# Kernel tuning notes

Hardware: AMD Instinct MI355X
Metric: run time of the kernel (lower is better)

## Reference

```python
import jax, jax.numpy as jnp
import numpy as np

B, D, QL, DL, E, V, NB = 32, 8, 16, 512, 300, 50000, 5
EPS = 1e-8  # torch cosine_similarity eps
# numpy.histogram edges [-1.0,-0.5,0,0.5,1.0,1.0] -> 5 bins, last bin [1.0,1.0] inclusive
BIN_LO = jnp.array([-1.0, -0.5, 0.0, 0.5, 1.0], dtype=jnp.float32)
BIN_HI = jnp.array([-0.5, 0.0, 0.5, 1.0, 1.0], dtype=jnp.float32)


def setup_inputs() -> dict:
    key = jax.random.key(0)
    ks = jax.random.split(key, 12)
    batch_queries = jax.random.randint(ks[0], (B, QL), 0, V)
    query_len = jax.random.randint(ks[1], (B,), 1, QL)
    batch_docs = jax.random.randint(ks[2], (B, D, DL), 0, V)
    doc_len = jax.random.randint(ks[3], (B, D), 1, DL)
    emb = jax.random.normal(ks[4], (V, E), dtype=jnp.float32) * 0.1
    emb = emb.at[0].set(0.0)  # PAD row (padding_idx)
    w_g = jax.random.normal(ks[5], (E, 1), dtype=jnp.float32) * 0.05
    b_g = jnp.zeros((1,), dtype=jnp.float32)
    w1 = jax.random.normal(ks[6], (NB, 1), dtype=jnp.float32) * 0.3
    b1 = jnp.zeros((1,), dtype=jnp.float32)
    w2 = jax.random.normal(ks[7], (1, 1), dtype=jnp.float32)
    b2 = jnp.zeros((1,), dtype=jnp.float32)
    w_o = jax.random.normal(ks[8], (1, 1), dtype=jnp.float32)
    b_o = jnp.zeros((1,), dtype=jnp.float32)
    return {"batch_queries": batch_queries, "query_len": query_len,
            "batch_docs": batch_docs, "doc_len": doc_len,
            "emb": emb, "w_g": w_g, "b_g": b_g, "w1": w1, "b1": b1,
            "w2": w2, "b2": b2, "w_o": w_o, "b_o": b_o}


def _histogram(cos):
    # cos: [N, qlen, dlen] -> counts [N, qlen, 5] (numpy.histogram semantics)
    v = cos[..., None]                              # [N,q,d,1]
    hi_ok = jnp.concatenate([v[..., :1] < BIN_HI[:4], v[..., :1] <= BIN_HI[4:]], axis=-1)
    mask = (v >= BIN_LO) & hi_ok                    # [N,q,d,5]
    return mask.astype(jnp.float32).sum(axis=2)     # [N,q,5]


def reference(batch_queries, query_len, batch_docs, doc_len,
              emb, w_g, b_g, w1, b1, w2, b2, w_o, b_o):
    q_emb = emb[batch_queries]                      # [B,q,E]
    # gating network: Linear(E,1) -> softmax over query terms
    gate = (q_emb @ w_g).squeeze(-1) + b_g          # [B,q]
    term_weights = jax.nn.softmax(gate, axis=1)     # [B,q]
    term_weights = jnp.broadcast_to(term_weights[:, None, :], (B, D, QL))

    d_emb = emb[batch_docs.reshape(B * D, DL)]      # [N,d,E]
    q_rep = jnp.broadcast_to(q_emb[:, None], (B, D, QL, E)).reshape(B * D, QL, E)

    # cosine similarity without materializing the replicated [N,q,d,E] tensors
    dots = jnp.einsum('nqe,nde->nqd', q_rep, d_emb)
    qn = jnp.linalg.norm(q_rep, axis=-1)            # [N,q]
    dn = jnp.linalg.norm(d_emb, axis=-1)            # [N,d]
    cos = dots / jnp.maximum(qn[:, :, None] * dn[:, None, :], EPS)

    # histogram feats are detached in the original (cpu numpy round-trip)
    hist = jax.lax.stop_gradient(_histogram(cos))   # [N,q,5]

    ffnn = ((hist @ w1 + b1) @ w2 + b2).squeeze(-1) # [N,q]
    ffnn = ffnn.reshape(B, D, QL)
    weighted = ffnn * term_weights                  # [B,D,q]
    s = weighted.sum(axis=2, keepdims=True)         # [B,D,1]
    score = (s @ w_o + b_o).squeeze(-1)             # [B,D]
    return score
```

## Files before the change

kernel.cpp:

```cpp
#include <hip/hip_runtime.h>


constexpr int Bn  = 32;
constexpr int Dn  = 8;
constexpr int QLn = 16;
constexpr int DLn = 512;
constexpr int En  = 300;

__global__ __launch_bounds__(256) void drmm_score(
    const int*   __restrict__ bq,
    const int*   __restrict__ bd,
    const float* __restrict__ emb,
    const float* __restrict__ w_g,
    const float* __restrict__ b_g,
    const float* __restrict__ w1,
    const float* __restrict__ b1,
    const float* __restrict__ w2,
    const float* __restrict__ b2,
    const float* __restrict__ w_o,
    const float* __restrict__ b_o,
    float*       __restrict__ out)
{
    __shared__ __attribute__((aligned(16))) float q_lds[QLn * En];
    __shared__ float pn_s[QLn][17];
    __shared__ float pg_s[QLn][17];
    __shared__ float qn_s[QLn];
    __shared__ float gate_s[QLn];
    __shared__ float tw_s[QLn];
    __shared__ unsigned long long hist_s[QLn];
    __shared__ float wsum_s[QLn];

    const int n   = blockIdx.x;
    const int b   = n >> 3;
    const int tid = threadIdx.x;

    for (int idx = tid; idx < QLn * En; idx += 256) {
        const int  q   = idx / En;
        const int  e   = idx - q * En;
        const long tok = bq[b * QLn + q];
        q_lds[idx] = emb[tok * (long)En + e];
    }
    if (tid < QLn) hist_s[tid] = 0ull;
    __syncthreads();

    {
        const int q = tid >> 4, j = tid & 15;
        float pn = 0.f, pg = 0.f;
        for (int e = j; e < En; e += 16) {
            const float v = q_lds[q * En + e];
            pn = fmaf(v, v, pn);
            pg = fmaf(v, w_g[e], pg);
        }
        pn_s[q][j] = pn;
        pg_s[q][j] = pg;
    }
    __syncthreads();
    if (tid < QLn) {
        float sn = 0.f, sg = 0.f;
        for (int j = 0; j < 16; ++j) { sn += pn_s[tid][j]; sg += pg_s[tid][j]; }
        qn_s[tid]   = sqrtf(sn);
        gate_s[tid] = sg + b_g[0];
    }
    __syncthreads();
    if (tid == 0) {
        float m = gate_s[0];
        for (int q = 1; q < QLn; ++q) m = fmaxf(m, gate_s[q]);
        float ex[QLn];
        float s = 0.f;
        for (int q = 0; q < QLn; ++q) { ex[q] = expf(gate_s[q] - m); s += ex[q]; }
        for (int q = 0; q < QLn; ++q) tw_s[q] = ex[q] / s;
    }
    __syncthreads();

    const long tok0 = bd[n * DLn + tid];
    const long tok1 = bd[n * DLn + tid + 256];
    const float* __restrict__ r0 = emb + tok0 * (long)En;
    const float* __restrict__ r1 = emb + tok1 * (long)En;

    float acc0[QLn], acc1[QLn];
#pragma unroll
    for (int q = 0; q < QLn; ++q) { acc0[q] = 0.f; acc1[q] = 0.f; }
    float nr0 = 0.f, nr1 = 0.f;

    float4 a0 = *reinterpret_cast<const float4*>(r0 + 0);
    float4 a1 = *reinterpret_cast<const float4*>(r1 + 0);
    float4 b0f = *reinterpret_cast<const float4*>(r0 + 4);
    float4 b1f = *reinterpret_cast<const float4*>(r1 + 4);

#define DRMM_COMPUTE(d0, d1, EE)                                          \
    do {                                                                  \
        nr0 = fmaf((d0).x, (d0).x, nr0);                                  \
        nr0 = fmaf((d0).y, (d0).y, nr0);                                  \
        nr0 = fmaf((d0).z, (d0).z, nr0);                                  \
        nr0 = fmaf((d0).w, (d0).w, nr0);                                  \
        nr1 = fmaf((d1).x, (d1).x, nr1);                                  \
        nr1 = fmaf((d1).y, (d1).y, nr1);                                  \
        nr1 = fmaf((d1).z, (d1).z, nr1);                                  \
        nr1 = fmaf((d1).w, (d1).w, nr1);                                  \
        _Pragma("unroll")                                                 \
        for (int q = 0; q < QLn; ++q) {                                   \
            const float4 qv =                                             \
                *reinterpret_cast<const float4*>(&q_lds[q * En + (EE)]);  \
            float s0 = acc0[q];                                           \
            s0 = fmaf((d0).x, qv.x, s0);                                  \
            s0 = fmaf((d0).y, qv.y, s0);                                  \
            s0 = fmaf((d0).z, qv.z, s0);                                  \
            s0 = fmaf((d0).w, qv.w, s0);                                  \
            acc0[q] = s0;                                                 \
            float s1 = acc1[q];                                           \
            s1 = fmaf((d1).x, qv.x, s1);                                  \
            s1 = fmaf((d1).y, qv.y, s1);                                  \
            s1 = fmaf((d1).z, qv.z, s1);                                  \
            s1 = fmaf((d1).w, qv.w, s1);                                  \
            acc1[q] = s1;                                                 \
        }                                                                 \
    } while (0)

    int e = 0;
    for (; e < En - 8; e += 4) {
        const float4 c0 = *reinterpret_cast<const float4*>(r0 + e + 8);
        const float4 c1 = *reinterpret_cast<const float4*>(r1 + e + 8);
        DRMM_COMPUTE(a0, a1, e);
        a0 = b0f; a1 = b1f;
        b0f = c0; b1f = c1;
    }
    DRMM_COMPUTE(a0, a1, 292);
    DRMM_COMPUTE(b0f, b1f, 296);
#undef DRMM_COMPUTE

    const float dn0 = sqrtf(nr0);
    const float dn1 = sqrtf(nr1);

    unsigned long long cnt[QLn];
#pragma unroll
    for (int q = 0; q < QLn; ++q) {
        unsigned long long v = 0ull;
        {
            const float denom = fmaxf(qn_s[q] * dn0, 1e-8f);
            const float c     = acc0[q] / denom;
            int bin = -1;
            if      (c >= -1.0f && c < -0.5f) bin = 0;
            else if (c >= -0.5f && c <  0.0f) bin = 1;
            else if (c >=  0.0f && c <  0.5f) bin = 2;
            else if (c >=  0.5f && c <  1.0f) bin = 3;
            else if (c ==  1.0f)              bin = 4;
            if (bin >= 0) v += 1ull << (12 * bin);
        }
        {
            const float denom = fmaxf(qn_s[q] * dn1, 1e-8f);
            const float c     = acc1[q] / denom;
            int bin = -1;
            if      (c >= -1.0f && c < -0.5f) bin = 0;
            else if (c >= -0.5f && c <  0.0f) bin = 1;
            else if (c >=  0.0f && c <  0.5f) bin = 2;
            else if (c >=  0.5f && c <  1.0f) bin = 3;
            else if (c ==  1.0f)              bin = 4;
            if (bin >= 0) v += 1ull << (12 * bin);
        }
        cnt[q] = v;
    }

    const int lane = tid & 63;
#pragma unroll
    for (int q = 0; q < QLn; ++q) {
        unsigned long long v = cnt[q];
        for (int off = 32; off > 0; off >>= 1) v += __shfl_down(v, off, 64);
        if (lane == 0) atomicAdd(&hist_s[q], v);
    }
    __syncthreads();

    if (tid < QLn) {
        const unsigned long long h = hist_s[tid];
        float f = 0.f;
        f = fmaf((float)((h >>  0) & 0xFFFull), w1[0], f);
        f = fmaf((float)((h >> 12) & 0xFFFull), w1[1], f);
        f = fmaf((float)((h >> 24) & 0xFFFull), w1[2], f);
        f = fmaf((float)((h >> 36) & 0xFFFull), w1[3], f);
        f = fmaf((float)((h >> 48) & 0xFFFull), w1[4], f);
        f += b1[0];
        f = f * w2[0] + b2[0];
        wsum_s[tid] = f * tw_s[tid];
    }
    __syncthreads();
    if (tid == 0) {
        float s = 0.f;
        for (int q = 0; q < QLn; ++q) s += wsum_s[q];
        out[n] = s * w_o[0] + b_o[0];
    }
}

extern "C" void kernel_launch(void* const* d_in, const int* in_sizes, int n_in,
                              void* d_out, int out_size, void* d_ws, size_t ws_size,
                              hipStream_t stream) {
    const int*   bq  = (const int*)  d_in[0];
    const int*   bd  = (const int*)  d_in[2];
    const float* emb = (const float*)d_in[4];
    const float* w_g = (const float*)d_in[5];
    const float* b_g = (const float*)d_in[6];
    const float* w1  = (const float*)d_in[7];
    const float* b1  = (const float*)d_in[8];
    const float* w2  = (const float*)d_in[9];
    const float* b2  = (const float*)d_in[10];
    const float* w_o = (const float*)d_in[11];
    const float* b_o = (const float*)d_in[12];

    drmm_score<<<Bn * Dn, 256, 0, stream>>>(
        bq, bd, emb, w_g, b_g, w1, b1, w2, b2, w_o, b_o, (float*)d_out);
}
```

Measured before the change: 70.78 us.

## Deepen doc-row prefetch to five float4 stages and vectorize query staging

The gather loop over each document embedding row now keeps five float4 loads per row in flight in a rotating register ring, where before it kept two. The outer loop is left un-unrolled over 20-element steps. The query embedding staging into LDS now uses float4 loads instead of scalar loads. The aim is to hide global gather latency in a latency-bound kernel, at the cost of extra registers that may reduce occupancy.

```diff
diff --git a/kernel.cpp b/kernel.cpp
--- a/kernel.cpp
+++ b/kernel.cpp
@@ -34,11 +34,12 @@
     const int b   = n >> 3;
     const int tid = threadIdx.x;
 
-    for (int idx = tid; idx < QLn * En; idx += 256) {
-        const int  q   = idx / En;
-        const int  e   = idx - q * En;
+    for (int idx = tid; idx < QLn * (En / 4); idx += 256) {
+        const int  q   = idx / (En / 4);
+        const int  c   = idx - q * (En / 4);
         const long tok = bq[b * QLn + q];
-        q_lds[idx] = emb[tok * (long)En + e];
+        *reinterpret_cast<float4*>(&q_lds[q * En + c * 4]) =
+            *reinterpret_cast<const float4*>(emb + tok * (long)En + c * 4);
     }
     if (tid < QLn) hist_s[tid] = 0ull;
     __syncthreads();
@@ -82,12 +83,7 @@
     for (int q = 0; q < QLn; ++q) { acc0[q] = 0.f; acc1[q] = 0.f; }
     float nr0 = 0.f, nr1 = 0.f;
 
-    float4 a0 = *reinterpret_cast<const float4*>(r0 + 0);
-    float4 a1 = *reinterpret_cast<const float4*>(r1 + 0);
-    float4 b0f = *reinterpret_cast<const float4*>(r0 + 4);
-    float4 b1f = *reinterpret_cast<const float4*>(r1 + 4);
-
-#define DRMM_COMPUTE(d0, d1, EE)                                          \
+#define DRMM_CHUNK(d0, d1, EE)                                            \
     do {                                                                  \
         nr0 = fmaf((d0).x, (d0).x, nr0);                                  \
         nr0 = fmaf((d0).y, (d0).y, nr0);                                  \
@@ -116,17 +112,40 @@
         }                                                                 \
     } while (0)
 
-    int e = 0;
-    for (; e < En - 8; e += 4) {
-        const float4 c0 = *reinterpret_cast<const float4*>(r0 + e + 8);
-        const float4 c1 = *reinterpret_cast<const float4*>(r1 + e + 8);
-        DRMM_COMPUTE(a0, a1, e);
-        a0 = b0f; a1 = b1f;
-        b0f = c0; b1f = c1;
-    }
-    DRMM_COMPUTE(a0, a1, 292);
-    DRMM_COMPUTE(b0f, b1f, 296);
-#undef DRMM_COMPUTE
+#define DRMM_STEP_R(SA, SB, EE)                                           \
+    do {                                                                  \
+        DRMM_CHUNK(SA, SB, (EE));                                         \
+        SA = *reinterpret_cast<const float4*>(r0 + (EE) + 20);            \
+        SB = *reinterpret_cast<const float4*>(r1 + (EE) + 20);            \
+    } while (0)
+
+    float4 s0a = *reinterpret_cast<const float4*>(r0 + 0);
+    float4 s1a = *reinterpret_cast<const float4*>(r1 + 0);
+    float4 s0b = *reinterpret_cast<const float4*>(r0 + 4);
+    float4 s1b = *reinterpret_cast<const float4*>(r1 + 4);
+    float4 s0c = *reinterpret_cast<const float4*>(r0 + 8);
+    float4 s1c = *reinterpret_cast<const float4*>(r1 + 8);
+    float4 s0d = *reinterpret_cast<const float4*>(r0 + 12);
+    float4 s1d = *reinterpret_cast<const float4*>(r1 + 12);
+    float4 s0e = *reinterpret_cast<const float4*>(r0 + 16);
+    float4 s1e = *reinterpret_cast<const float4*>(r1 + 16);
+
+#pragma unroll 1
+    for (int k = 0; k < 14; ++k) {
+        const int e = k * 20;
+        DRMM_STEP_R(s0a, s1a, e + 0);
+        DRMM_STEP_R(s0b, s1b, e + 4);
+        DRMM_STEP_R(s0c, s1c, e + 8);
+        DRMM_STEP_R(s0d, s1d, e + 12);
+        DRMM_STEP_R(s0e, s1e, e + 16);
+    }
+    DRMM_CHUNK(s0a, s1a, 280);
+    DRMM_CHUNK(s0b, s1b, 284);
+    DRMM_CHUNK(s0c, s1c, 288);
+    DRMM_CHUNK(s0d, s1d, 292);
+    DRMM_CHUNK(s0e, s1e, 296);
+#undef DRMM_STEP_R
+#undef DRMM_CHUNK
 
     const float dn0 = sqrtf(nr0);
     const float dn1 = sqrtf(nr1);
```

Result: faster. 60.17 us (-15.0%).
